# Optimization experiments

Hardware: AMD Instinct MI355X
Metric: run time of the kernel (lower is better)

## Reference

```python
import jax, jax.numpy as jnp
import numpy as np

NUM_TAGS = 5

def setup_inputs() -> dict:
    key = jax.random.key(0)
    ks = jax.random.split(key, 8)
    B, N, K, Q = 2, 5, 5, 4
    Ls, Lq, D = 128, 128, 768
    inp = {
        'support_token_embedding': jax.random.normal(ks[0], (B * N * K, Ls, D), jnp.float32),
        'query_token_embedding': jax.random.normal(ks[1], (B * N * Q, Lq, D), jnp.float32),
        'support_mask': jnp.ones((B * N * K, Ls), jnp.float32),
        'query_mask': jnp.ones((B * N * Q, Lq), jnp.float32),
        'support_entity_label': jax.random.normal(ks[2], (B * N * K, Ls, NUM_TAGS), jnp.float32),
        'proj_w': jax.random.normal(ks[3], (D, 4 * D), jnp.float32) * 0.02,
        'proj_b': jnp.zeros((D,), jnp.float32),
        'rel_w1': jax.random.normal(ks[4], (D, 4 * D), jnp.float32) * 0.02,
        'rel_b1': jnp.zeros((D,), jnp.float32),
        'rel_w2': jax.random.normal(ks[5], (1, D), jnp.float32) * 0.02,
        'rel_b2': jnp.zeros((1,), jnp.float32),
        'B': B, 'N': N, 'K': K, 'Q': Q,
    }
    return inp

def _fuse(m1, m2):
    return jnp.concatenate([m1, m2, jnp.abs(m1 - m2), m1 * m2], axis=-1)

def reference(support_token_embedding, query_token_embedding, support_mask, query_mask,
              support_entity_label, proj_w, proj_b, rel_w1, rel_b1, rel_w2, rel_b2,
              B, N, K, Q):
    D = support_token_embedding.shape[-1]
    Lq = query_token_embedding.shape[1]

    # ---- cal_bio: per-(sample,shot) tag prototypes, vectorized ----
    labels = jnp.argmax(support_entity_label, axis=-1)                 # [BNK, Ls]
    onehot = jax.nn.one_hot(labels, NUM_TAGS, dtype=jnp.float32)       # [BNK, Ls, T]
    # tag 0 ('O') is additionally gated by the support mask
    masks = jnp.concatenate([onehot[:, :, :1] * support_mask[:, :, None], onehot[:, :, 1:]], axis=2)
    sums = jnp.einsum('blt,bld->btd', masks, support_token_embedding)  # [BNK, T, D]
    cnt = jnp.sum(masks, axis=1)[:, :, None]                           # [BNK, T, 1]
    proto = jnp.where(cnt > 0, sums / jnp.maximum(cnt, 1.0), 0.0)      # [BNK, T, D]
    proto = proto.reshape(B * N, K, NUM_TAGS, D).mean(axis=1)          # mean over K shots
    proto = proto.reshape(B, N, NUM_TAGS, D)                           # support_BIO

    # ---- expand to all (query, class) pairs: batch = B*N*Q*N ----
    BQ = B * N * Q * N
    support = jnp.broadcast_to(proto[:, None], (B, N * Q, N, NUM_TAGS, D)).reshape(BQ, NUM_TAGS, D)
    query = jnp.broadcast_to(query_token_embedding.reshape(B, N * Q, 1, Lq, D),
                             (B, N * Q, N, Lq, D)).reshape(BQ, Lq, D)
    qmask = jnp.broadcast_to(query_mask.reshape(B, N * Q, 1, Lq),
                             (B, N * Q, N, Lq)).reshape(BQ, Lq, 1)
    smask = jnp.ones((BQ, NUM_TAGS, 1), jnp.float32)

    # ---- CoAttention with additive mask bias + post-softmax mask multiply ----
    att = jnp.einsum('bsd,bqd->bsq', support, query) + smask * jnp.swapaxes(qmask, 1, 2) * 100.0
    support_ = jnp.einsum('bsq,bqd->bsd', jax.nn.softmax(att, axis=2), query) * smask
    query_ = jnp.einsum('bqs,bsd->bqd', jax.nn.softmax(jnp.swapaxes(att, 1, 2), axis=2), support) * qmask

    # ---- fuse + proj + relu ----
    es = jax.nn.relu(_fuse(support, support_) @ proj_w.T + proj_b)     # [BQ, T, D]
    eq = jax.nn.relu(_fuse(query, query_) @ proj_w.T + proj_b)        # [BQ, Lq, D]

    # ---- local aggregation: masked max + mean pooling ----
    eq_agg = jnp.concatenate([jnp.max(eq, axis=1), jnp.sum(eq, axis=1) / jnp.sum(qmask, axis=1)], axis=1)
    es_agg = jnp.concatenate([jnp.max(es, axis=1), jnp.sum(es, axis=1) / jnp.sum(smask, axis=1)], axis=1)

    # ---- relation MLP ----
    cat_seq = jnp.concatenate([eq_agg, es_agg], axis=1)                # [BQ, 4D]
    h = jax.nn.relu(cat_seq @ rel_w1.T + rel_b1)
    logits = h @ rel_w2.T + rel_b2                                     # [BQ, 1]
    return logits.reshape(B * N * Q, N)
```

## Files before the change

### kernel.cpp

```cpp
#include <hip/hip_runtime.h>

typedef unsigned short u16;
typedef __attribute__((ext_vector_type(8))) short short8;
typedef __attribute__((ext_vector_type(4))) float f32x4;

#define B_   2
#define N_   5
#define K_   5
#define Q_   4
#define T_   5
#define D_   768
#define L_   128
#define BN_  (B_*N_)
#define BNK_ (B_*N_*K_)
#define BQ_  (B_*N_*Q_*N_)
#define K4_  (4*D_)
#define KFQ  1536
#define AROWS 144

#define QEMB_N  (40*128*768)
#define PROJW_N (768*3072)

__device__ __forceinline__ float bf2f(u16 u) {
    return __uint_as_float(((unsigned)u) << 16);
}
__device__ __forceinline__ u16 f2bf(float f) {
    unsigned u = __float_as_uint(f);
    return (u16)((u + 0x7fffu + ((u >> 16) & 1u)) >> 16);
}
__device__ __forceinline__ void gl_lds16(const u16* g, u16* l) {
    __builtin_amdgcn_global_load_lds(
        (const __attribute__((address_space(1))) unsigned int*)g,
        (__attribute__((address_space(3))) unsigned int*)l, 16, 0, 0);
}

__global__ void k_convert3(const float* __restrict__ q, const float* __restrict__ pw,
                           const float* __restrict__ rw, u16* __restrict__ qo,
                           u16* __restrict__ po, u16* __restrict__ ro) {
    const long n1 = QEMB_N / 4, n2 = PROJW_N / 4;
    const long total = n1 + 2 * n2;
    for (long i = (long)blockIdx.x * 256 + threadIdx.x; i < total; i += (long)gridDim.x * 256) {
        const float* src; u16* dst; long k;
        if (i < n1)            { src = q;  dst = qo; k = i; }
        else if (i < n1 + n2)  { src = pw; dst = po; k = i - n1; }
        else                   { src = rw; dst = ro; k = i - n1 - n2; }
        float4 v = ((const float4*)src)[k];
        u16 o[4] = {f2bf(v.x), f2bf(v.y), f2bf(v.z), f2bf(v.w)};
        *(uint2*)(dst + k * 4) = *(const uint2*)o;
    }
}

__global__ void k_proto_shot(const float* __restrict__ label, const float* __restrict__ smask,
                             const float* __restrict__ semb, float* __restrict__ proto_shot) {
    int bnk = blockIdx.x;
    __shared__ int   s_tag[L_];
    __shared__ float s_w[L_];
    __shared__ float s_cnt[T_];
    int tid = threadIdx.x;
    if (tid < L_) {
        const float* lp = label + ((long)bnk * L_ + tid) * T_;
        float best = lp[0]; int bi = 0;
        #pragma unroll
        for (int t = 1; t < T_; ++t) { float v = lp[t]; if (v > best) { best = v; bi = t; } }
        s_tag[tid] = bi;
        s_w[tid]   = (bi == 0) ? smask[(long)bnk * L_ + tid] : 1.0f;
    }
    __syncthreads();
    if (tid < T_) {
        float c = 0.f;
        for (int l = 0; l < L_; ++l) if (s_tag[l] == tid) c += s_w[l];
        s_cnt[tid] = c;
    }
    __syncthreads();
    float acc[3][T_] = {};
    for (int l = 0; l < L_; ++l) {
        float w = s_w[l]; int tg = s_tag[l];
        const float* ep = semb + ((long)bnk * L_ + l) * D_;
        #pragma unroll
        for (int s = 0; s < 3; ++s) {
            float e = ep[tid + s * 256] * w;
            #pragma unroll
            for (int t = 0; t < T_; ++t) acc[s][t] += (tg == t) ? e : 0.0f;
        }
    }
    #pragma unroll
    for (int s = 0; s < 3; ++s) {
        int d = tid + s * 256;
        #pragma unroll
        for (int t = 0; t < T_; ++t) {
            float c = s_cnt[t];
            float v = (c > 0.f) ? acc[s][t] / fmaxf(c, 1.f) : 0.f;
            proto_shot[(bnk * T_ + t) * D_ + d] = v;
        }
    }
}

__global__ void k_proto_mean(const float* __restrict__ proto_shot,
                             float* __restrict__ proto_f32, u16* __restrict__ proto_bf) {
    int idx = blockIdx.x * 256 + threadIdx.x;
    if (idx >= BN_ * T_ * D_) return;
    int bn = idx / (T_ * D_);
    int rem = idx - bn * (T_ * D_);
    float s = 0.f;
    #pragma unroll
    for (int k = 0; k < K_; ++k) s += proto_shot[(bn * K_ + k) * (T_ * D_) + rem];
    s *= (1.f / K_);
    proto_f32[idx] = s;
    proto_bf[idx]  = f2bf(s);
}

__global__ void k_attn(const float* __restrict__ qemb, const float* __restrict__ qmask_g,
                       const float* __restrict__ proto_f32,
                       u16* __restrict__ qf, u16* __restrict__ sup_ws,
                       float* __restrict__ p2m_ws, float* __restrict__ qssum_ws) {
    int x = blockIdx.x;
    int xcd = x & 7, slot = x >> 3;
    int g = (slot / 5) * 8 + xcd;
    int n2 = slot % 5;
    int bq = g * 5 + n2;
    int q_idx = g;
    int bn = (bq / (N_ * Q_ * N_)) * N_ + (bq % N_);
    __shared__ float s_proto[T_ * D_];
    __shared__ float s_att[T_][L_];
    __shared__ float s_ps[T_][L_];
    __shared__ float s_p2[L_][8];
    __shared__ float s_qm[L_];
    int tid = threadIdx.x;
    int w = tid >> 6, lane = tid & 63;
    for (int i = tid; i < T_ * D_; i += 256) s_proto[i] = proto_f32[bn * T_ * D_ + i];
    if (tid < L_) s_qm[tid] = qmask_g[(long)q_idx * L_ + tid];
    __syncthreads();
    for (int p = tid; p < T_ * L_; p += 256) {
        int t = p >> 7, q = p & (L_ - 1);
        const float* pp = s_proto + t * D_;
        const float4* qp = (const float4*)(qemb + ((size_t)q_idx * L_ + q) * D_);
        float acc = 0.f;
        #pragma unroll 4
        for (int d = 0; d < D_ / 4; ++d) {
            float4 v = qp[d];
            acc += v.x * pp[4 * d] + v.y * pp[4 * d + 1] + v.z * pp[4 * d + 2] + v.w * pp[4 * d + 3];
        }
        s_att[t][q] = acc + 100.f * s_qm[q];
    }
    __syncthreads();
    if (tid < T_) {
        int t = tid; float m = -1e30f;
        for (int q = 0; q < L_; ++q) m = fmaxf(m, s_att[t][q]);
        float ss = 0.f;
        for (int q = 0; q < L_; ++q) { float e = __expf(s_att[t][q] - m); s_ps[t][q] = e; ss += e; }
        float inv = 1.f / ss;
        for (int q = 0; q < L_; ++q) s_ps[t][q] *= inv;
    } else if (tid >= 128) {
        int q = tid - 128; float m = -1e30f;
        float e[T_];
        #pragma unroll
        for (int t = 0; t < T_; ++t) m = fmaxf(m, s_att[t][q]);
        float ss = 0.f;
        #pragma unroll
        for (int t = 0; t < T_; ++t) { e[t] = __expf(s_att[t][q] - m); ss += e[t]; }
        float inv = s_qm[q] / ss;
        #pragma unroll
        for (int t = 0; t < T_; ++t) {
            s_p2[q][t] = e[t] * inv;
            p2m_ws[((size_t)bq * T_ + t) * L_ + q] = e[t] * inv;
        }
    } else if (tid == 5) {
        float s = 0.f;
        for (int q = 0; q < L_; ++q) s += s_qm[q];
        qssum_ws[bq] = s;
    }
    __syncthreads();
    u16* qfb = qf + (size_t)bq * AROWS * KFQ;
    {
        float acc[T_][3] = {};
        #pragma unroll 4
        for (int q = 0; q < L_; ++q) {
            const float* qp = qemb + ((size_t)q_idx * L_ + q) * D_;
            float qv[3];
            #pragma unroll
            for (int s = 0; s < 3; ++s) qv[s] = qp[tid + s * 256];
            #pragma unroll
            for (int t = 0; t < T_; ++t) {
                float p = s_ps[t][q];
                #pragma unroll
                for (int s = 0; s < 3; ++s) acc[t][s] += p * qv[s];
            }
        }
        #pragma unroll
        for (int t = 0; t < T_; ++t) {
            u16* er = qfb + (size_t)(128 + t) * KFQ;
            #pragma unroll
            for (int s = 0; s < 3; ++s) {
                int d = tid + s * 256;
                float p = s_proto[t * D_ + d];
                float sv = acc[t][s];
                sup_ws[((size_t)bq * T_ + t) * D_ + d] = f2bf(sv);
                er[d]       = f2bf(fabsf(p - sv));
                er[768 + d] = f2bf(p * sv);
            }
        }
    }
    for (int rr = 0; rr < 32; ++rr) {
        int row = w * 32 + rr;
        float p0 = s_p2[row][0], p1 = s_p2[row][1], p2v = s_p2[row][2];
        float p3 = s_p2[row][3], p4 = s_p2[row][4];
        const float* qrow = qemb + ((size_t)q_idx * L_ + row) * D_;
        u16* qr = qfb + (size_t)row * KFQ;
        #pragma unroll
        for (int pass = 0; pass < 2; ++pass) {
            int u = lane + pass * 64;
            if (u < 96) {
                int d = u * 8;
                float4 a0 = *(const float4*)(qrow + d);
                float4 a1 = *(const float4*)(qrow + d + 4);
                float qv[8] = {a0.x, a0.y, a0.z, a0.w, a1.x, a1.y, a1.z, a1.w};
                short8 o2, o3;
                #pragma unroll
                for (int i = 0; i < 8; ++i) {
                    float m2 = p0 * s_proto[d + i] + p1 * s_proto[D_ + d + i]
                             + p2v * s_proto[2 * D_ + d + i] + p3 * s_proto[3 * D_ + d + i]
                             + p4 * s_proto[4 * D_ + d + i];
                    o2[i] = (short)f2bf(fabsf(qv[i] - m2));
                    o3[i] = (short)f2bf(qv[i] * m2);
                }
                *(short8*)(qr + d)       = o2;
                *(short8*)(qr + 768 + d) = o3;
            }
        }
    }
    {
        u16* pr = qfb + (size_t)133 * KFQ;
        short8 z = short8{0, 0, 0, 0, 0, 0, 0, 0};
        for (int i = tid; i < (11 * KFQ) / 8; i += 256) *(short8*)(pr + i * 8) = z;
    }
}

#define SWZ(g, r) (((g) << 4) + ((r) ^ ((g) << 2)))
__global__ __launch_bounds__(256) void k_gemm_g1(const u16* __restrict__ qemb_bf,
                                                 const u16* __restrict__ proto_bf,
                                                 const u16* __restrict__ projw_bf,
                                                 u16* __restrict__ g1) {
    int mbase = blockIdx.y * 128;
    int jbase = blockIdx.x * 128;
    __shared__ __align__(16) u16 sA[8 * 512];
    __shared__ __align__(16) u16 sB[8 * 512];
    int tid = threadIdx.x;
    int lane = tid & 63, w = tid >> 6, quad = lane >> 4, l16 = lane & 15;
    f32x4 zero = {0.f, 0.f, 0.f, 0.f};
    f32x4 acc[8][2];
    #pragma unroll
    for (int rt = 0; rt < 8; ++rt) { acc[rt][0] = zero; acc[rt][1] = zero; }

    for (int kt = 0; kt < 24; ++kt) {
        int k0 = kt * 32;
        __syncthreads();
        #pragma unroll
        for (int j = 0; j < 2; ++j) {
            int v = tid + j * 256, row = v >> 2, g = v & 3;
            *(uint4*)(sB + (((row >> 4) << 6) + SWZ(g, row & 15)) * 8) =
                *(const uint4*)(projw_bf + (size_t)(jbase + row) * K4_ + k0 + g * 8);
            int grow = mbase + row;
            uint4 av = uint4{0u, 0u, 0u, 0u};
            if (grow < 5120)      av = *(const uint4*)(qemb_bf + (size_t)grow * D_ + k0 + g * 8);
            else if (grow < 5170) av = *(const uint4*)(proto_bf + (size_t)(grow - 5120) * D_ + k0 + g * 8);
            *(uint4*)(sA + (((row >> 4) << 6) + SWZ(g, row & 15)) * 8) = av;
        }
        __syncthreads();
        short8 af[8], bfr[2];
        #pragma unroll
        for (int rt = 0; rt < 8; ++rt)
            af[rt] = *(const short8*)(sA + ((rt << 6) + SWZ(quad, l16)) * 8);
        #pragma unroll
        for (int jj = 0; jj < 2; ++jj)
            bfr[jj] = *(const short8*)(sB + (((w * 2 + jj) << 6) + SWZ(quad, l16)) * 8);
        #pragma unroll
        for (int rt = 0; rt < 8; ++rt)
            #pragma unroll
            for (int jj = 0; jj < 2; ++jj)
                acc[rt][jj] = __builtin_amdgcn_mfma_f32_16x16x32_bf16(af[rt], bfr[jj], acc[rt][jj], 0, 0, 0);
    }
    #pragma unroll
    for (int jj = 0; jj < 2; ++jj) {
        int col = jbase + (w * 2 + jj) * 16 + l16;
        #pragma unroll
        for (int rt = 0; rt < 8; ++rt)
            #pragma unroll
            for (int r = 0; r < 4; ++r) {
                int row = mbase + rt * 16 + quad * 4 + r;
                g1[(size_t)row * D_ + col] = f2bf(acc[rt][jj][r]);
            }
    }
}

__global__ __launch_bounds__(256) void k_gemm_w2(const u16* __restrict__ sup_ws,
                                                 const u16* __restrict__ proto_bf,
                                                 const u16* __restrict__ projw_bf,
                                                 u16* __restrict__ sw2, u16* __restrict__ pw2) {
    int mbase = blockIdx.y * 128;
    int jbase = blockIdx.x * 128;
    __shared__ __align__(16) u16 sA[8 * 512];
    __shared__ __align__(16) u16 sB[8 * 512];
    int tid = threadIdx.x;
    int lane = tid & 63, w = tid >> 6, quad = lane >> 4, l16 = lane & 15;
    f32x4 zero = {0.f, 0.f, 0.f, 0.f};
    f32x4 acc[8][2];
    #pragma unroll
    for (int rt = 0; rt < 8; ++rt) { acc[rt][0] = zero; acc[rt][1] = zero; }

    for (int kt = 0; kt < 24; ++kt) {
        int k0 = kt * 32;
        __syncthreads();
        #pragma unroll
        for (int j = 0; j < 2; ++j) {
            int v = tid + j * 256, row = v >> 2, g = v & 3;
            *(uint4*)(sB + (((row >> 4) << 6) + SWZ(g, row & 15)) * 8) =
                *(const uint4*)(projw_bf + (size_t)(jbase + row) * K4_ + 768 + k0 + g * 8);
            int grow = mbase + row;
            uint4 av = uint4{0u, 0u, 0u, 0u};
            if (grow < 1000)      av = *(const uint4*)(sup_ws + (size_t)grow * D_ + k0 + g * 8);
            else if (grow < 1050) av = *(const uint4*)(proto_bf + (size_t)(grow - 1000) * D_ + k0 + g * 8);
            *(uint4*)(sA + (((row >> 4) << 6) + SWZ(g, row & 15)) * 8) = av;
        }
        __syncthreads();
        short8 af[8], bfr[2];
        #pragma unroll
        for (int rt = 0; rt < 8; ++rt)
            af[rt] = *(const short8*)(sA + ((rt << 6) + SWZ(quad, l16)) * 8);
        #pragma unroll
        for (int jj = 0; jj < 2; ++jj)
            bfr[jj] = *(const short8*)(sB + (((w * 2 + jj) << 6) + SWZ(quad, l16)) * 8);
        #pragma unroll
        for (int rt = 0; rt < 8; ++rt)
            #pragma unroll
            for (int jj = 0; jj < 2; ++jj)
                acc[rt][jj] = __builtin_amdgcn_mfma_f32_16x16x32_bf16(af[rt], bfr[jj], acc[rt][jj], 0, 0, 0);
    }
    #pragma unroll
    for (int jj = 0; jj < 2; ++jj) {
        int col = jbase + (w * 2 + jj) * 16 + l16;
        #pragma unroll
        for (int rt = 0; rt < 8; ++rt)
            #pragma unroll
            for (int r = 0; r < 4; ++r) {
                int row = mbase + rt * 16 + quad * 4 + r;
                if (row < 1000)      sw2[(size_t)row * D_ + col] = f2bf(acc[rt][jj][r]);
                else if (row < 1050) pw2[(size_t)(row - 1000) * D_ + col] = f2bf(acc[rt][jj][r]);
            }
    }
}

__global__ __launch_bounds__(256) void k_gemm_q(
        const u16* __restrict__ qf, const u16* __restrict__ projw_bf,
        const float* __restrict__ projb, const u16* __restrict__ g1,
        const u16* __restrict__ pw2, const u16* __restrict__ sw2,
        const float* __restrict__ p2m, const float* __restrict__ qssum_ws,
        u16* __restrict__ cat_ws) {
    int x = blockIdx.x;
    int xcd = x & 7, slot = x >> 3;
    int bq = (slot / 6) * 8 + xcd;
    int jbase = (slot % 6) * 128;
    int q_idx = bq / N_;
    int bn = (bq / (N_ * Q_ * N_)) * N_ + (bq % N_);
    __shared__ __align__(16) u16 sT[2][(AROWS + 128) * 32];
    __shared__ float s_p2mL[T_ * 128];
    __shared__ float s_pw2L[T_ * 128];
    int tid = threadIdx.x;
    int lane = tid & 63, w = tid >> 6, quad = lane >> 4, l16 = lane & 15;
    int srow = lane >> 2, sko = lane & 3;
    const u16* Ab = qf + ((size_t)bq * AROWS + srow) * KFQ + sko * 8;
    const u16* Bb = projw_bf + (size_t)(jbase + srow) * K4_ + 1536 + sko * 8;

    f32x4 zero = {0.f, 0.f, 0.f, 0.f};
    f32x4 acc[9][2];
    #pragma unroll
    for (int rt = 0; rt < 9; ++rt) { acc[rt][0] = zero; acc[rt][1] = zero; }

    auto issue = [&](int kt, int b) {
        int k0 = kt * 32;
        u16* base = sT[b];
        gl_lds16(Ab + (size_t)(w * 16) * KFQ + k0, base + (w * 16) * 32);
        gl_lds16(Ab + (size_t)(64 + w * 16) * KFQ + k0, base + (64 + w * 16) * 32);
        if (w == 0) gl_lds16(Ab + (size_t)128 * KFQ + k0, base + 128 * 32);
        gl_lds16(Bb + (size_t)(w * 16) * K4_ + k0, base + (AROWS + w * 16) * 32);
        gl_lds16(Bb + (size_t)(64 + w * 16) * K4_ + k0, base + (AROWS + 64 + w * 16) * 32);
    };

    issue(0, 0);
    for (int kt = 0; kt < KFQ / 32; ++kt) {
        int cur = kt & 1;
        __syncthreads();
        if (kt + 1 < KFQ / 32) issue(kt + 1, 1 - cur);
        const u16* base = sT[cur];
        short8 af[9], bfr[2];
        #pragma unroll
        for (int rt = 0; rt < 9; ++rt)
            af[rt] = *(const short8*)(base + (rt * 16 + l16) * 32 + quad * 8);
        #pragma unroll
        for (int jj = 0; jj < 2; ++jj)
            bfr[jj] = *(const short8*)(base + (AROWS + (w * 2 + jj) * 16 + l16) * 32 + quad * 8);
        #pragma unroll
        for (int rt = 0; rt < 9; ++rt)
            #pragma unroll
            for (int jj = 0; jj < 2; ++jj)
                acc[rt][jj] = __builtin_amdgcn_mfma_f32_16x16x32_bf16(af[rt], bfr[jj], acc[rt][jj], 0, 0, 0);
    }
    for (int i = tid; i < T_ * 128; i += 256) {
        s_p2mL[i] = p2m[(size_t)bq * (T_ * 128) + i];
        s_pw2L[i] = bf2f(pw2[(size_t)(bn * T_ + (i >> 7)) * D_ + jbase + (i & 127)]);
    }
    __syncthreads();
    float inv_qs = 1.f / qssum_ws[bq];
    #pragma unroll
    for (int jj = 0; jj < 2; ++jj) {
        int col = jbase + (w * 2 + jj) * 16 + l16;
        int cj = (w * 2 + jj) * 16 + l16;
        float bias = projb[col];
        float qmax = 0.f, qsum = 0.f, smax = 0.f, ssum = 0.f;
        #pragma unroll
        for (int rt = 0; rt < 8; ++rt) {
            #pragma unroll
            for (int r = 0; r < 4; ++r) {
                int row = rt * 16 + quad * 4 + r;
                float g1v = bf2f(g1[(size_t)(q_idx * 128 + row) * D_ + col]);
                float mix = s_p2mL[row] * s_pw2L[cj]
                          + s_p2mL[128 + row] * s_pw2L[128 + cj]
                          + s_p2mL[256 + row] * s_pw2L[256 + cj]
                          + s_p2mL[384 + row] * s_pw2L[384 + cj]
                          + s_p2mL[512 + row] * s_pw2L[512 + cj];
                float v = fmaxf(acc[rt][jj][r] + g1v + mix + bias, 0.f);
                qmax = fmaxf(qmax, v); qsum += v;
            }
        }
        #pragma unroll
        for (int r = 0; r < 4; ++r) {
            int t = quad * 4 + r;
            if (t < T_) {
                float g1v = bf2f(g1[(size_t)(5120 + bn * T_ + t) * D_ + col]);
                float s2v = bf2f(sw2[(size_t)(bq * T_ + t) * D_ + col]);
                float v = fmaxf(acc[8][jj][r] + g1v + s2v + bias, 0.f);
                smax = fmaxf(smax, v); ssum += v;
            }
        }
        qmax = fmaxf(qmax, __shfl_xor(qmax, 16, 64)); qmax = fmaxf(qmax, __shfl_xor(qmax, 32, 64));
        qsum += __shfl_xor(qsum, 16, 64);             qsum += __shfl_xor(qsum, 32, 64);
        smax = fmaxf(smax, __shfl_xor(smax, 16, 64)); smax = fmaxf(smax, __shfl_xor(smax, 32, 64));
        ssum += __shfl_xor(ssum, 16, 64);             ssum += __shfl_xor(ssum, 32, 64);
        if (quad == 0) {
            u16* cp = cat_ws + (size_t)bq * K4_;
            cp[col]           = f2bf(qmax);
            cp[D_ + col]      = f2bf(qsum * inv_qs);
            cp[2 * D_ + col]  = f2bf(smax);
            cp[3 * D_ + col]  = f2bf(ssum * 0.2f);
        }
    }
}

#define AST  40
__global__ __launch_bounds__(256) void k_relmlp(const u16* __restrict__ cat_ws,
                                                const u16* __restrict__ w1,
                                                float* __restrict__ part) {
    int mbase = blockIdx.y * 64;
    int jbase = blockIdx.x * 128;
    int ks = blockIdx.z;
    __shared__ __align__(16) u16 sA[64 * AST];
    __shared__ __align__(16) u16 sB[128 * AST];
    int tid = threadIdx.x;
    int lane = tid & 63, w = tid >> 6, quad = lane >> 4, l16 = lane & 15;
    f32x4 zero = {0.f, 0.f, 0.f, 0.f};
    f32x4 acc[4][2];
    #pragma unroll
    for (int rt = 0; rt < 4; ++rt) { acc[rt][0] = zero; acc[rt][1] = zero; }

    for (int kt = ks * 12; kt < ks * 12 + 12; ++kt) {
        int k0 = kt * 32;
        __syncthreads();
        {
            int row = tid >> 2, ko = (tid & 3) * 8;
            int grow = mbase + row;
            short8 val = short8{0, 0, 0, 0, 0, 0, 0, 0};
            if (grow < BQ_) val = *(const short8*)(cat_ws + (size_t)grow * K4_ + k0 + ko);
            *(short8*)(sA + row * AST + ko) = val;
        }
        for (int u = tid; u < 512; u += 256) {
            int row = u >> 2, ko = (u & 3) * 8;
            *(short8*)(sB + row * AST + ko) =
                *(const short8*)(w1 + (size_t)(jbase + row) * K4_ + k0 + ko);
        }
        __syncthreads();
        short8 af[4], bfr[2];
        #pragma unroll
        for (int rt = 0; rt < 4; ++rt)
            af[rt] = *(const short8*)(sA + (rt * 16 + l16) * AST + quad * 8);
        #pragma unroll
        for (int jj = 0; jj < 2; ++jj)
            bfr[jj] = *(const short8*)(sB + ((2 * w + jj) * 16 + l16) * AST + quad * 8);
        #pragma unroll
        for (int rt = 0; rt < 4; ++rt)
            #pragma unroll
            for (int jj = 0; jj < 2; ++jj)
                acc[rt][jj] = __builtin_amdgcn_mfma_f32_16x16x32_bf16(af[rt], bfr[jj], acc[rt][jj], 0, 0, 0);
    }
    #pragma unroll
    for (int jj = 0; jj < 2; ++jj) {
        int col = jbase + (2 * w + jj) * 16 + l16;
        #pragma unroll
        for (int rt = 0; rt < 4; ++rt) {
            #pragma unroll
            for (int r = 0; r < 4; ++r) {
                int grow = mbase + rt * 16 + quad * 4 + r;
                if (grow < BQ_)
                    part[((size_t)ks * BQ_ + grow) * D_ + col] = acc[rt][jj][r];
            }
        }
    }
}

__global__ void k_rel_fin(const float* __restrict__ part, const float* __restrict__ b1,
                          const float* __restrict__ w2, const float* __restrict__ b2,
                          float* __restrict__ out) {
    int bq = blockIdx.x, tid = threadIdx.x;
    float a = 0.f;
    #pragma unroll
    for (int s = 0; s < 3; ++s) {
        int col = tid + s * 256;
        float sum = 0.f;
        #pragma unroll
        for (int ks = 0; ks < 8; ++ks) sum += part[((size_t)ks * BQ_ + bq) * D_ + col];
        float h = fmaxf(sum + b1[col], 0.f);
        a += h * w2[col];
    }
    __shared__ float red[256];
    red[tid] = a; __syncthreads();
    for (int off = 128; off >= 1; off >>= 1) {
        if (tid < off) red[tid] += red[tid + off];
        __syncthreads();
    }
    if (tid == 0) out[bq] = red[0] + b2[0];
}

extern "C" void kernel_launch(void* const* d_in, const int* in_sizes, int n_in,
                              void* d_out, int out_size, void* d_ws, size_t ws_size,
                              hipStream_t stream) {
    (void)in_sizes; (void)n_in; (void)out_size; (void)ws_size;
    const float* semb  = (const float*)d_in[0];
    const float* qemb  = (const float*)d_in[1];
    const float* smask = (const float*)d_in[2];
    const float* qmask = (const float*)d_in[3];
    const float* label = (const float*)d_in[4];
    const float* projw = (const float*)d_in[5];
    const float* projb = (const float*)d_in[6];
    const float* relw1 = (const float*)d_in[7];
    const float* relb1 = (const float*)d_in[8];
    const float* relw2 = (const float*)d_in[9];
    const float* relb2 = (const float*)d_in[10];

    char* ws = (char*)d_ws;
    u16*   qemb_bf   = (u16*)  (ws + 0);
    u16*   projw_bf  = (u16*)  (ws + 7864320);
    u16*   relw1_bf  = (u16*)  (ws + 12582912);
    float* proto_shot= (float*)(ws + 17301504);
    float* proto_f32 = (float*)(ws + 18069504);
    u16*   proto_bf  = (u16*)  (ws + 18223104);
    float* qssum     = (float*)(ws + 18299904);
    u16*   sup_ws    = (u16*)  (ws + 18300800);
    float* p2m_ws    = (float*)(ws + 19836800);
    u16*   pw2_ws    = (u16*)  (ws + 20348800);
    u16*   sw2_ws    = (u16*)  (ws + 20425600);
    u16*   cat_ws    = (u16*)  (ws + 21961600);
    u16*   g1_ws     = (u16*)  (ws + 23190400);
    float* part_ws   = (float*)(ws + 31251328);
    u16*   qf_ws     = (u16*)  (ws + 36166528);

    k_convert3<<<2048, 256, 0, stream>>>(qemb, projw, relw1, qemb_bf, projw_bf, relw1_bf);
    k_proto_shot<<<BNK_, 256, 0, stream>>>(label, smask, semb, proto_shot);
    k_proto_mean<<<150, 256, 0, stream>>>(proto_shot, proto_f32, proto_bf);
    k_attn<<<BQ_, 256, 0, stream>>>(qemb, qmask, proto_f32, qf_ws, sup_ws, p2m_ws, qssum);
    k_gemm_g1<<<dim3(6, 41), 256, 0, stream>>>(qemb_bf, proto_bf, projw_bf, g1_ws);
    k_gemm_w2<<<dim3(6, 9), 256, 0, stream>>>(sup_ws, proto_bf, projw_bf, sw2_ws, pw2_ws);
    k_gemm_q<<<1200, 256, 0, stream>>>(qf_ws, projw_bf, projb, g1_ws, pw2_ws, sw2_ws,
                                       p2m_ws, qssum, cat_ws);
    k_relmlp<<<dim3(6, 4, 8), 256, 0, stream>>>(cat_ws, relw1_bf, part_ws);
    k_rel_fin<<<BQ_, 256, 0, stream>>>(part_ws, relb1, relw2, relb2, (float*)d_out);
}
```

Before: 531.7 us.

## Split proto and query GEMM work across more blocks and restage qf epilogue

k_proto_shot now launches three blocks per support sample, one per 256-column slice of D, so more CUs share the work. k_gemm_q halves its column tile from 128 to 64 and doubles the grid to 2400 blocks with a launch-bounds occupancy hint of 3. This shrinks accumulators and LDS per block but reloads the A tile twice as often. k_attn's abs-diff/product feature write now stages m2 through shared memory in 32-column slabs, giving coalesced per-element qemb reads and qf writes, at the cost of extra barriers and 16-bit scalar stores in place of vector stores.

```diff
diff --git a/kernel.cpp b/kernel.cpp
--- a/kernel.cpp
+++ b/kernel.cpp
@@ -53,6 +53,7 @@
 __global__ void k_proto_shot(const float* __restrict__ label, const float* __restrict__ smask,
                              const float* __restrict__ semb, float* __restrict__ proto_shot) {
     int bnk = blockIdx.x;
+    int s = blockIdx.y;
     __shared__ int   s_tag[L_];
     __shared__ float s_w[L_];
     __shared__ float s_cnt[T_];
@@ -72,26 +73,19 @@
         s_cnt[tid] = c;
     }
     __syncthreads();
-    float acc[3][T_] = {};
+    float acc[T_] = {};
     for (int l = 0; l < L_; ++l) {
         float w = s_w[l]; int tg = s_tag[l];
-        const float* ep = semb + ((long)bnk * L_ + l) * D_;
-        #pragma unroll
-        for (int s = 0; s < 3; ++s) {
-            float e = ep[tid + s * 256] * w;
-            #pragma unroll
-            for (int t = 0; t < T_; ++t) acc[s][t] += (tg == t) ? e : 0.0f;
-        }
-    }
-    #pragma unroll
-    for (int s = 0; s < 3; ++s) {
-        int d = tid + s * 256;
-        #pragma unroll
-        for (int t = 0; t < T_; ++t) {
-            float c = s_cnt[t];
-            float v = (c > 0.f) ? acc[s][t] / fmaxf(c, 1.f) : 0.f;
-            proto_shot[(bnk * T_ + t) * D_ + d] = v;
-        }
+        float e = semb[((long)bnk * L_ + l) * D_ + tid + s * 256] * w;
+        #pragma unroll
+        for (int t = 0; t < T_; ++t) acc[t] += (tg == t) ? e : 0.0f;
+    }
+    int d = tid + s * 256;
+    #pragma unroll
+    for (int t = 0; t < T_; ++t) {
+        float c = s_cnt[t];
+        float v = (c > 0.f) ? acc[t] / fmaxf(c, 1.f) : 0.f;
+        proto_shot[(bnk * T_ + t) * D_ + d] = v;
     }
 }
 
@@ -125,8 +119,8 @@
     __shared__ float s_ps[T_][L_];
     __shared__ float s_p2[L_][8];
     __shared__ float s_qm[L_];
+    __shared__ float s_m2[L_][33];
     int tid = threadIdx.x;
-    int w = tid >> 6, lane = tid & 63;
     for (int i = tid; i < T_ * D_; i += 256) s_proto[i] = proto_f32[bn * T_ * D_ + i];
     if (tid < L_) s_qm[tid] = qmask_g[(long)q_idx * L_ + tid];
     __syncthreads();
@@ -200,38 +194,40 @@
             }
         }
     }
-    for (int rr = 0; rr < 32; ++rr) {
-        int row = w * 32 + rr;
-        float p0 = s_p2[row][0], p1 = s_p2[row][1], p2v = s_p2[row][2];
-        float p3 = s_p2[row][3], p4 = s_p2[row][4];
-        const float* qrow = qemb + ((size_t)q_idx * L_ + row) * D_;
-        u16* qr = qfb + (size_t)row * KFQ;
-        #pragma unroll
-        for (int pass = 0; pass < 2; ++pass) {
-            int u = lane + pass * 64;
-            if (u < 96) {
-                int d = u * 8;
-                float4 a0 = *(const float4*)(qrow + d);
-                float4 a1 = *(const float4*)(qrow + d + 4);
-                float qv[8] = {a0.x, a0.y, a0.z, a0.w, a1.x, a1.y, a1.z, a1.w};
-                short8 o2, o3;
-                #pragma unroll
-                for (int i = 0; i < 8; ++i) {
-                    float m2 = p0 * s_proto[d + i] + p1 * s_proto[D_ + d + i]
-                             + p2v * s_proto[2 * D_ + d + i] + p3 * s_proto[3 * D_ + d + i]
-                             + p4 * s_proto[4 * D_ + d + i];
-                    o2[i] = (short)f2bf(fabsf(qv[i] - m2));
-                    o3[i] = (short)f2bf(qv[i] * m2);
-                }
-                *(short8*)(qr + d)       = o2;
-                *(short8*)(qr + 768 + d) = o3;
-            }
-        }
-    }
     {
-        u16* pr = qfb + (size_t)133 * KFQ;
+        int row_b = tid & 127, half = tid >> 7;
+        float pr[T_];
+        #pragma unroll
+        for (int t = 0; t < T_; ++t) pr[t] = s_p2[row_b][t];
+        int d2 = tid & 31, r0 = tid >> 5;
+        for (int slab = 0; slab < 24; ++slab) {
+            #pragma unroll
+            for (int j = 0; j < 16; ++j) {
+                int col = half * 16 + j;
+                int d = slab * 32 + col;
+                float m2 = pr[0] * s_proto[d] + pr[1] * s_proto[D_ + d]
+                         + pr[2] * s_proto[2 * D_ + d] + pr[3] * s_proto[3 * D_ + d]
+                         + pr[4] * s_proto[4 * D_ + d];
+                s_m2[row_b][col] = m2;
+            }
+            __syncthreads();
+            #pragma unroll
+            for (int k = 0; k < 16; ++k) {
+                int row = r0 + k * 8;
+                int dd = slab * 32 + d2;
+                float m2 = s_m2[row][d2];
+                float qv = qemb[((size_t)q_idx * L_ + row) * D_ + dd];
+                u16* qr = qfb + (size_t)row * KFQ;
+                qr[dd]        = f2bf(fabsf(qv - m2));
+                qr[768 + dd]  = f2bf(qv * m2);
+            }
+            __syncthreads();
+        }
+    }
+    {
+        u16* pr2 = qfb + (size_t)133 * KFQ;
         short8 z = short8{0, 0, 0, 0, 0, 0, 0, 0};
-        for (int i = tid; i < (11 * KFQ) / 8; i += 256) *(short8*)(pr + i * 8) = z;
+        for (int i = tid; i < (11 * KFQ) / 8; i += 256) *(short8*)(pr2 + i * 8) = z;
     }
 }
 
@@ -349,7 +345,7 @@
     }
 }
 
-__global__ __launch_bounds__(256) void k_gemm_q(
+__global__ __launch_bounds__(256, 3) void k_gemm_q(
         const u16* __restrict__ qf, const u16* __restrict__ projw_bf,
         const float* __restrict__ projb, const u16* __restrict__ g1,
         const u16* __restrict__ pw2, const u16* __restrict__ sw2,
@@ -357,13 +353,13 @@
         u16* __restrict__ cat_ws) {
     int x = blockIdx.x;
     int xcd = x & 7, slot = x >> 3;
-    int bq = (slot / 6) * 8 + xcd;
-    int jbase = (slot % 6) * 128;
+    int bq = (slot / 12) * 8 + xcd;
+    int jbase = (slot % 12) * 64;
     int q_idx = bq / N_;
     int bn = (bq / (N_ * Q_ * N_)) * N_ + (bq % N_);
-    __shared__ __align__(16) u16 sT[2][(AROWS + 128) * 32];
+    __shared__ __align__(16) u16 sT[2][(AROWS + 64) * 32];
     __shared__ float s_p2mL[T_ * 128];
-    __shared__ float s_pw2L[T_ * 128];
+    __shared__ float s_pw2L[T_ * 64];
     int tid = threadIdx.x;
     int lane = tid & 63, w = tid >> 6, quad = lane >> 4, l16 = lane & 15;
     int srow = lane >> 2, sko = lane & 3;
@@ -371,9 +367,9 @@
     const u16* Bb = projw_bf + (size_t)(jbase + srow) * K4_ + 1536 + sko * 8;
 
     f32x4 zero = {0.f, 0.f, 0.f, 0.f};
-    f32x4 acc[9][2];
-    #pragma unroll
-    for (int rt = 0; rt < 9; ++rt) { acc[rt][0] = zero; acc[rt][1] = zero; }
+    f32x4 acc[9];
+    #pragma unroll
+    for (int rt = 0; rt < 9; ++rt) acc[rt] = zero;
 
     auto issue = [&](int kt, int b) {
         int k0 = kt * 32;
@@ -382,7 +378,6 @@
         gl_lds16(Ab + (size_t)(64 + w * 16) * KFQ + k0, base + (64 + w * 16) * 32);
         if (w == 0) gl_lds16(Ab + (size_t)128 * KFQ + k0, base + 128 * 32);
         gl_lds16(Bb + (size_t)(w * 16) * K4_ + k0, base + (AROWS + w * 16) * 32);
-        gl_lds16(Bb + (size_t)(64 + w * 16) * K4_ + k0, base + (AROWS + 64 + w * 16) * 32);
     };
 
     issue(0, 0);
@@ -391,29 +386,23 @@
         __syncthreads();
         if (kt + 1 < KFQ / 32) issue(kt + 1, 1 - cur);
         const u16* base = sT[cur];
-        short8 af[9], bfr[2];
+        short8 af[9], bf1;
         #pragma unroll
         for (int rt = 0; rt < 9; ++rt)
             af[rt] = *(const short8*)(base + (rt * 16 + l16) * 32 + quad * 8);
-        #pragma unroll
-        for (int jj = 0; jj < 2; ++jj)
-            bfr[jj] = *(const short8*)(base + (AROWS + (w * 2 + jj) * 16 + l16) * 32 + quad * 8);
+        bf1 = *(const short8*)(base + (AROWS + w * 16 + l16) * 32 + quad * 8);
         #pragma unroll
         for (int rt = 0; rt < 9; ++rt)
-            #pragma unroll
-            for (int jj = 0; jj < 2; ++jj)
-                acc[rt][jj] = __builtin_amdgcn_mfma_f32_16x16x32_bf16(af[rt], bfr[jj], acc[rt][jj], 0, 0, 0);
-    }
-    for (int i = tid; i < T_ * 128; i += 256) {
-        s_p2mL[i] = p2m[(size_t)bq * (T_ * 128) + i];
-        s_pw2L[i] = bf2f(pw2[(size_t)(bn * T_ + (i >> 7)) * D_ + jbase + (i & 127)]);
-    }
+            acc[rt] = __builtin_amdgcn_mfma_f32_16x16x32_bf16(af[rt], bf1, acc[rt], 0, 0, 0);
+    }
+    for (int i = tid; i < T_ * 128; i += 256) s_p2mL[i] = p2m[(size_t)bq * (T_ * 128) + i];
+    for (int i = tid; i < T_ * 64; i += 256)
+        s_pw2L[i] = bf2f(pw2[(size_t)(bn * T_ + (i >> 6)) * D_ + jbase + (i & 63)]);
     __syncthreads();
     float inv_qs = 1.f / qssum_ws[bq];
-    #pragma unroll
-    for (int jj = 0; jj < 2; ++jj) {
-        int col = jbase + (w * 2 + jj) * 16 + l16;
-        int cj = (w * 2 + jj) * 16 + l16;
+    {
+        int c = w * 16 + l16;
+        int col = jbase + c;
         float bias = projb[col];
         float qmax = 0.f, qsum = 0.f, smax = 0.f, ssum = 0.f;
         #pragma unroll
@@ -422,12 +411,12 @@
             for (int r = 0; r < 4; ++r) {
                 int row = rt * 16 + quad * 4 + r;
                 float g1v = bf2f(g1[(size_t)(q_idx * 128 + row) * D_ + col]);
-                float mix = s_p2mL[row] * s_pw2L[cj]
-                          + s_p2mL[128 + row] * s_pw2L[128 + cj]
-                          + s_p2mL[256 + row] * s_pw2L[256 + cj]
-                          + s_p2mL[384 + row] * s_pw2L[384 + cj]
-                          + s_p2mL[512 + row] * s_pw2L[512 + cj];
-                float v = fmaxf(acc[rt][jj][r] + g1v + mix + bias, 0.f);
+                float mix = s_p2mL[row] * s_pw2L[c]
+                          + s_p2mL[128 + row] * s_pw2L[64 + c]
+                          + s_p2mL[256 + row] * s_pw2L[128 + c]
+                          + s_p2mL[384 + row] * s_pw2L[192 + c]
+                          + s_p2mL[512 + row] * s_pw2L[256 + c];
+                float v = fmaxf(acc[rt][r] + g1v + mix + bias, 0.f);
                 qmax = fmaxf(qmax, v); qsum += v;
             }
         }
@@ -437,7 +426,7 @@
             if (t < T_) {
                 float g1v = bf2f(g1[(size_t)(5120 + bn * T_ + t) * D_ + col]);
                 float s2v = bf2f(sw2[(size_t)(bq * T_ + t) * D_ + col]);
-                float v = fmaxf(acc[8][jj][r] + g1v + s2v + bias, 0.f);
+                float v = fmaxf(acc[8][r] + g1v + s2v + bias, 0.f);
                 smax = fmaxf(smax, v); ssum += v;
             }
         }
@@ -572,12 +561,12 @@
     u16*   qf_ws     = (u16*)  (ws + 36166528);
 
     k_convert3<<<2048, 256, 0, stream>>>(qemb, projw, relw1, qemb_bf, projw_bf, relw1_bf);
-    k_proto_shot<<<BNK_, 256, 0, stream>>>(label, smask, semb, proto_shot);
+    k_proto_shot<<<dim3(BNK_, 3), 256, 0, stream>>>(label, smask, semb, proto_shot);
     k_proto_mean<<<150, 256, 0, stream>>>(proto_shot, proto_f32, proto_bf);
     k_attn<<<BQ_, 256, 0, stream>>>(qemb, qmask, proto_f32, qf_ws, sup_ws, p2m_ws, qssum);
     k_gemm_g1<<<dim3(6, 41), 256, 0, stream>>>(qemb_bf, proto_bf, projw_bf, g1_ws);
     k_gemm_w2<<<dim3(6, 9), 256, 0, stream>>>(sup_ws, proto_bf, projw_bf, sw2_ws, pw2_ws);
-    k_gemm_q<<<1200, 256, 0, stream>>>(qf_ws, projw_bf, projb, g1_ws, pw2_ws, sw2_ws,
+    k_gemm_q<<<2400, 256, 0, stream>>>(qf_ws, projw_bf, projb, g1_ws, pw2_ws, sw2_ws,
                                        p2m_ws, qssum, cat_ws);
     k_relmlp<<<dim3(6, 4, 8), 256, 0, stream>>>(cat_ws, relw1_bf, part_ws);
     k_rel_fin<<<BQ_, 256, 0, stream>>>(part_ws, relb1, relw2, relb2, (float*)d_out);
```

Result: no change. 535.9 us (+0.8%).
